# Performance work log

Measured on AMD Instinct MI355X. Metric: run time of the kernel, lower is better.

Reference implementation:

```python
import jax, jax.numpy as jnp
import numpy as np

BETA = 0.99  # EMA momentum from init_kwargs
EPS = 1e-12  # torch F.normalize eps


def _normalize(v):
    # matches torch.nn.functional.normalize (L2, dim=-1, eps clamp)
    n = jnp.maximum(jnp.linalg.norm(v, axis=-1, keepdims=True), EPS)
    return v / n


def setup_inputs() -> dict:
    key = jax.random.key(0)
    k1, k2 = jax.random.split(key)
    x = jax.random.normal(k1, (16384, 1024), dtype=jnp.float32)
    group_features = jax.random.uniform(k2, (8192, 1024), dtype=jnp.float32)
    return {"x": x, "group_features": group_features}


def reference(x, group_features):
    n_groups = group_features.shape[0]
    # assign_groups: cosine-sim argmax (normalized copies; does NOT modify x used below)
    xn = _normalize(x)
    gn = _normalize(group_features)
    logits = xn @ gn.T                      # [B, G]
    assignments = jnp.argmax(logits, axis=-1)  # [B] int

    # bincount over groups
    counts = jax.ops.segment_sum(
        jnp.ones_like(assignments, dtype=jnp.int32), assignments, num_segments=n_groups
    )  # [G]

    # scale only groups that received at least one sample by beta
    gf = jnp.where((counts > 0)[:, None], group_features * BETA, group_features)

    # scatter-add EMA contribution: (1-beta) * mean-style sum of raw x per group
    per_sample = x / counts[assignments][:, None].astype(x.dtype)  # safe: count>=1 for assigned
    contrib = jax.ops.segment_sum(per_sample, assignments, num_segments=n_groups)  # [G, D]
    gf = gf + (1.0 - BETA) * contrib

    return _normalize(gf)
```

## Files before the change

### kernel.cpp

```cpp
#include <hip/hip_runtime.h>
#include <float.h>

#define B_N 16384
#define G_N 8192
#define D_N 1024
#define NKT 48

typedef unsigned short u16;
typedef unsigned long long u64;
typedef __attribute__((ext_vector_type(8))) short short8;
typedef __attribute__((ext_vector_type(4))) float f32x4;

#define AS1 __attribute__((address_space(1)))
#define AS3 __attribute__((address_space(3)))


__global__ __launch_bounds__(256) void k_norms(const float* __restrict__ g,
                                               float* __restrict__ invn) {
    const int j = blockIdx.x;
    const int t = threadIdx.x;
    const float4 v = *reinterpret_cast<const float4*>(&g[(size_t)j * D_N + t * 4]);
    float s = v.x * v.x + v.y * v.y + v.z * v.z + v.w * v.w;
#pragma unroll
    for (int off = 32; off >= 1; off >>= 1) s += __shfl_down(s, off, 64);
    __shared__ float wsum[4];
    if ((t & 63) == 0) wsum[t >> 6] = s;
    __syncthreads();
    if (t == 0) {
        const float tot = wsum[0] + wsum[1] + wsum[2] + wsum[3];
        invn[j] = 1.0f / fmaxf(sqrtf(tot), 1e-12f);
    }
}

__global__ void k_counts(const u64* __restrict__ pk, int* __restrict__ counts) {
    const int i = blockIdx.x * blockDim.x + threadIdx.x;
    if (i < B_N) {
        const int a = 8191 - (int)(pk[i] & 0x1FFFull);
        atomicAdd(&counts[a], 1);
    }
}

__global__ __launch_bounds__(256) void k_scatter(const float* __restrict__ x,
                                                 const u64* __restrict__ pk,
                                                 const int* __restrict__ counts,
                                                 float* __restrict__ contrib) {
    const int i = blockIdx.x;
    const int a = 8191 - (int)(pk[i] & 0x1FFFull);
    const float scale = 1.0f / (float)counts[a];
    const int t = threadIdx.x;
    const float4 v = *reinterpret_cast<const float4*>(&x[(size_t)i * D_N + t * 4]);
    float* dst = &contrib[(size_t)a * D_N + t * 4];
    atomicAdd(dst + 0, v.x * scale);
    atomicAdd(dst + 1, v.y * scale);
    atomicAdd(dst + 2, v.z * scale);
    atomicAdd(dst + 3, v.w * scale);
}

__global__ __launch_bounds__(256) void k_finalize(const float* __restrict__ g,
                                                  const int* __restrict__ counts,
                                                  float* __restrict__ out) {
    const int j = blockIdx.x;
    const int t = threadIdx.x;
    const float sc = (counts[j] > 0) ? 0.99f : 1.0f;
    const float4 gv = *reinterpret_cast<const float4*>(&g[(size_t)j * D_N + t * 4]);
    const float4 cv = *reinterpret_cast<const float4*>(&out[(size_t)j * D_N + t * 4]);
    float4 gf;
    gf.x = sc * gv.x + 0.01f * cv.x;
    gf.y = sc * gv.y + 0.01f * cv.y;
    gf.z = sc * gv.z + 0.01f * cv.z;
    gf.w = sc * gv.w + 0.01f * cv.w;
    float s = gf.x * gf.x + gf.y * gf.y + gf.z * gf.z + gf.w * gf.w;
#pragma unroll
    for (int off = 32; off >= 1; off >>= 1) s += __shfl_down(s, off, 64);
    __shared__ float wsum[4];
    __shared__ float s_inv;
    if ((t & 63) == 0) wsum[t >> 6] = s;
    __syncthreads();
    if (t == 0) s_inv = 1.0f / fmaxf(sqrtf(wsum[0] + wsum[1] + wsum[2] + wsum[3]), 1e-12f);
    __syncthreads();
    gf.x *= s_inv; gf.y *= s_inv; gf.z *= s_inv; gf.w *= s_inv;
    *reinterpret_cast<float4*>(&out[(size_t)j * D_N + t * 4]) = gf;
}


__device__ inline u16 f2bf_rtn(float f) {
    unsigned u = __float_as_uint(f);
    unsigned r = u + 0x7fffu + ((u >> 16) & 1u);
    return (u16)(r >> 16);
}
__device__ inline float bf2f(u16 h) { return __uint_as_float(((unsigned)h) << 16); }

__global__ __launch_bounds__(256) void k_split(const float* __restrict__ src,
                                               u16* __restrict__ hi,
                                               u16* __restrict__ lo) {
    const size_t i4 = (size_t)blockIdx.x * 256 + threadIdx.x;
    const float4 v = *reinterpret_cast<const float4*>(&src[i4 * 4]);
    u16 h[4], l[4];
    const float f[4] = {v.x, v.y, v.z, v.w};
#pragma unroll
    for (int j = 0; j < 4; ++j) {
        h[j] = f2bf_rtn(f[j]);
        l[j] = f2bf_rtn(f[j] - bf2f(h[j]));
    }
    *reinterpret_cast<ushort4*>(&hi[i4 * 4]) = make_ushort4(h[0], h[1], h[2], h[3]);
    *reinterpret_cast<ushort4*>(&lo[i4 * 4]) = make_ushort4(l[0], l[1], l[2], l[3]);
}


#define PHASE(BUFI, Q, READB, STG, DOVM) do {                                              \
    const u16* aL = lds + (BUFI) * 32768;                                                  \
    const u16* bL = aL + 16384;                                                            \
    _Pragma("unroll")                                                                      \
    for (int dm = 0; dm < 2; ++dm) {                                                       \
        const u16* fb = aL + (wr * 8 + (Q) * 2 + dm) * 1024;                               \
        afr[dm][0] = *reinterpret_cast<const short8*>(fb + aoff0);                         \
        afr[dm][1] = *reinterpret_cast<const short8*>(fb + aoff1);                         \
    }                                                                                      \
    if (READB) {                                                                           \
        _Pragma("unroll")                                                                  \
        for (int n = 0; n < 4; ++n) {                                                      \
            const u16* fb = bL + (wc * 4 + n) * 1024;                                      \
            bfr[n][0] = *reinterpret_cast<const short8*>(fb + aoff0);                      \
            bfr[n][1] = *reinterpret_cast<const short8*>(fb + aoff1);                      \
        }                                                                                  \
    }                                                                                      \
    STG;                                                                                   \
    if (DOVM) asm volatile("s_waitcnt vmcnt(6)" ::: "memory");                             \
    __builtin_amdgcn_s_barrier();                                                          \
    asm volatile("s_waitcnt lgkmcnt(0)" ::: "memory");                                     \
    __builtin_amdgcn_s_setprio(1);                                                         \
    _Pragma("unroll")                                                                      \
    for (int s = 0; s < 2; ++s)                                                            \
        _Pragma("unroll")                                                                  \
        for (int dm = 0; dm < 2; ++dm)                                                     \
            _Pragma("unroll")                                                              \
            for (int n = 0; n < 4; ++n)                                                    \
                acc[(Q) * 2 + dm][n] = __builtin_amdgcn_mfma_f32_16x16x32_bf16(            \
                    afr[dm][s], bfr[n][s], acc[(Q) * 2 + dm][n], 0, 0, 0);                 \
    __builtin_amdgcn_s_setprio(0);                                                         \
    __builtin_amdgcn_s_barrier();                                                          \
} while (0)

__global__ __launch_bounds__(512, 2) void k_gemm_argmax(
    const u16* __restrict__ x_hi, const u16* __restrict__ x_lo,
    const u16* __restrict__ g_hi, const u16* __restrict__ g_lo,
    const float* __restrict__ invn, u64* __restrict__ pk) {

    __shared__ __align__(16) u16 lds[65536];

    const int bid = blockIdx.x;
    const int xcd = bid & 7, lcl = bid >> 3;
    const int mblk = xcd * 8 + (lcl >> 5);
    const int nblk = lcl & 31;

    const int tid = threadIdx.x;
    const int lane = tid & 63;
    const int w = tid >> 6;
    const int wr = w >> 2, wc = w & 3;
    const int mrow0 = mblk * 256;
    const int nrow0 = nblk * 256;

    const int rl = lane & 15, kg = lane >> 4;
    const int xr = rl & 7;
    const int sl0 = kg ^ xr;
    const int aoff0 = rl * 64 + (sl0 << 3);
    const int aoff1 = rl * 64 + ((sl0 ^ 4) << 3);

    const size_t soff0 = (size_t)(tid >> 3) * D_N + (size_t)(((tid & 7) ^ ((tid >> 3) & 7)) * 8);
    const size_t soff1 = soff0 + (size_t)64 * D_N;
    const int wub = (tid & 448) * 8;

    auto STGA = [&](int ktx, int half) {
        int kt = ktx < NKT ? ktx : NKT - 1;
        const u16* base = (kt >= 16 && kt < 32) ? x_lo : x_hi;
        const u16* s0 = base + (size_t)(mrow0 + half * 128) * D_N + (kt & 15) * 64;
        u16* dreg = lds + (kt & 1) * 32768 + half * 8192;
        __builtin_amdgcn_global_load_lds((const AS1 void*)(s0 + soff0), (AS3 void*)(dreg + wub), 16, 0, 0);
        __builtin_amdgcn_global_load_lds((const AS1 void*)(s0 + soff1), (AS3 void*)(dreg + wub + 4096), 16, 0, 0);
    };
    auto STGB = [&](int ktx, int half) {
        int kt = ktx < NKT ? ktx : NKT - 1;
        const u16* base = (kt < 32) ? g_hi : g_lo;
        const u16* s0 = base + (size_t)(nrow0 + half * 128) * D_N + (kt & 15) * 64;
        u16* dreg = lds + (kt & 1) * 32768 + 16384 + half * 8192;
        __builtin_amdgcn_global_load_lds((const AS1 void*)(s0 + soff0), (AS3 void*)(dreg + wub), 16, 0, 0);
        __builtin_amdgcn_global_load_lds((const AS1 void*)(s0 + soff1), (AS3 void*)(dreg + wub + 4096), 16, 0, 0);
    };

    f32x4 acc[8][4];
#pragma unroll
    for (int m = 0; m < 8; ++m)
#pragma unroll
        for (int n = 0; n < 4; ++n) acc[m][n] = (f32x4){0.f, 0.f, 0.f, 0.f};
    short8 afr[2][2], bfr[4][2];

    STGB(0, 0); STGB(0, 1); STGA(0, 0); STGA(0, 1);
    STGB(1, 0); STGB(1, 1); STGA(1, 0);
    asm volatile("s_waitcnt vmcnt(6)" ::: "memory");
    __builtin_amdgcn_s_barrier();

    for (int kt0 = 0; kt0 < NKT; kt0 += 2) {
        const int kt1 = kt0 + 1;
        PHASE(0, 0, true,  STGA(kt1, 1),     false);
        PHASE(0, 1, false, STGB(kt0 + 2, 0), false);
        PHASE(0, 2, false, STGB(kt0 + 2, 1), false);
        PHASE(0, 3, false, STGA(kt0 + 2, 0), true);
        PHASE(1, 0, true,  STGA(kt0 + 2, 1), false);
        PHASE(1, 1, false, STGB(kt1 + 2, 0), false);
        PHASE(1, 2, false, STGB(kt1 + 2, 1), false);
        PHASE(1, 3, false, STGA(kt1 + 2, 0), true);
    }

    float inv[4];
#pragma unroll
    for (int n = 0; n < 4; ++n) inv[n] = invn[nrow0 + wc * 64 + n * 16 + rl];

#pragma unroll
    for (int m = 0; m < 8; ++m) {
#pragma unroll
        for (int j = 0; j < 4; ++j) {
            u64 p = 0;
#pragma unroll
            for (int n = 0; n < 4; ++n) {
                const float v = acc[m][n][j] * inv[n];
                unsigned u = __float_as_uint(v);
                u ^= (u >> 31) ? 0xFFFFFFFFu : 0x80000000u;
                const int col = nrow0 + wc * 64 + n * 16 + rl;
                const u64 cand = ((u64)u << 13) | (unsigned)(8191 - col);
                p = (cand > p) ? cand : p;
            }
#pragma unroll
            for (int msk = 1; msk < 16; msk <<= 1) {
                const u64 o = __shfl_xor(p, msk, 64);
                p = (o > p) ? o : p;
            }
            if (rl == 0) {
                const int row = mrow0 + wr * 128 + m * 16 + kg * 4 + j;
                atomicMax(&pk[row], p);
            }
        }
    }
}


__global__ __launch_bounds__(256) void k_argmax_fp32(const float* __restrict__ x,
                                                     const float* __restrict__ g,
                                                     const float* __restrict__ invn,
                                                     int* __restrict__ assign) {
    __shared__ __align__(16) float As[32][68];
    __shared__ __align__(16) float Bs[32][68];
    const int t = threadIdx.x;
    const int tx = t & 15;
    const int ty = t >> 4;
    const int row0 = blockIdx.x * 64;
    const int r_a = t >> 3;
    const int c4 = t & 7;
    float bestv[4]; int besti[4];
#pragma unroll
    for (int i = 0; i < 4; ++i) { bestv[i] = -3.0e38f; besti[i] = 0; }
    for (int jt = 0; jt < G_N / 64; ++jt) {
        float acc[4][4] = {};
        for (int kt = 0; kt < D_N / 32; ++kt) {
#pragma unroll
            for (int p = 0; p < 2; ++p) {
                const int r = r_a + p * 32;
                const float4 va = *reinterpret_cast<const float4*>(&x[(size_t)(row0 + r) * D_N + kt * 32 + c4 * 4]);
                As[c4 * 4 + 0][r] = va.x; As[c4 * 4 + 1][r] = va.y; As[c4 * 4 + 2][r] = va.z; As[c4 * 4 + 3][r] = va.w;
                const float4 vb = *reinterpret_cast<const float4*>(&g[(size_t)(jt * 64 + r) * D_N + kt * 32 + c4 * 4]);
                Bs[c4 * 4 + 0][r] = vb.x; Bs[c4 * 4 + 1][r] = vb.y; Bs[c4 * 4 + 2][r] = vb.z; Bs[c4 * 4 + 3][r] = vb.w;
            }
            __syncthreads();
#pragma unroll
            for (int k = 0; k < 32; ++k) {
                const float4 a = *reinterpret_cast<const float4*>(&As[k][ty * 4]);
                const float4 b = *reinterpret_cast<const float4*>(&Bs[k][tx * 4]);
                const float av[4] = {a.x, a.y, a.z, a.w};
                const float bv[4] = {b.x, b.y, b.z, b.w};
#pragma unroll
                for (int i = 0; i < 4; ++i)
#pragma unroll
                    for (int jj = 0; jj < 4; ++jj) acc[i][jj] += av[i] * bv[jj];
            }
            __syncthreads();
        }
#pragma unroll
        for (int jj = 0; jj < 4; ++jj) {
            const int col = jt * 64 + tx * 4 + jj;
            const float s = invn[col];
#pragma unroll
            for (int i = 0; i < 4; ++i) {
                const float v = acc[i][jj] * s;
                if (v > bestv[i]) { bestv[i] = v; besti[i] = col; }
            }
        }
    }
#pragma unroll
    for (int m = 1; m < 16; m <<= 1) {
#pragma unroll
        for (int i = 0; i < 4; ++i) {
            const float ov = __shfl_xor(bestv[i], m, 64);
            const int oi = __shfl_xor(besti[i], m, 64);
            if (ov > bestv[i] || (ov == bestv[i] && oi < besti[i])) { bestv[i] = ov; besti[i] = oi; }
        }
    }
    if (tx == 0) {
#pragma unroll
        for (int i = 0; i < 4; ++i) assign[row0 + ty * 4 + i] = besti[i];
    }
}

__global__ void k_counts_i(const int* __restrict__ assign, int* __restrict__ counts) {
    const int i = blockIdx.x * blockDim.x + threadIdx.x;
    if (i < B_N) atomicAdd(&counts[assign[i]], 1);
}

__global__ __launch_bounds__(256) void k_scatter_i(const float* __restrict__ x,
                                                   const int* __restrict__ assign,
                                                   const int* __restrict__ counts,
                                                   float* __restrict__ contrib) {
    const int i = blockIdx.x;
    const int a = assign[i];
    const float scale = 1.0f / (float)counts[a];
    const int t = threadIdx.x;
    const float4 v = *reinterpret_cast<const float4*>(&x[(size_t)i * D_N + t * 4]);
    float* dst = &contrib[(size_t)a * D_N + t * 4];
    atomicAdd(dst + 0, v.x * scale);
    atomicAdd(dst + 1, v.y * scale);
    atomicAdd(dst + 2, v.z * scale);
    atomicAdd(dst + 3, v.w * scale);
}


extern "C" void kernel_launch(void* const* d_in, const int* in_sizes, int n_in,
                              void* d_out, int out_size, void* d_ws, size_t ws_size,
                              hipStream_t stream) {
    const float* x = (const float*)d_in[0];
    const float* g = (const float*)d_in[1];
    float* out = (float*)d_out;

    char* ws = (char*)d_ws;
    u16*  x_hi  = (u16*)(ws);
    u16*  x_lo  = (u16*)(ws + 33554432);
    u16*  g_hi  = (u16*)(ws + 67108864);
    u16*  g_lo  = (u16*)(ws + 83886080);
    float* invn = (float*)(ws + 100663296);
    int* counts = (int*)(ws + 100696064);
    u64*   pk   = (u64*)(ws + 100728832);
    const size_t need = 100859904;

    hipMemsetAsync(out, 0, (size_t)G_N * D_N * sizeof(float), stream);

    if (ws_size >= need) {
        hipMemsetAsync(counts, 0, (size_t)G_N * sizeof(int), stream);
        hipMemsetAsync(pk, 0, (size_t)B_N * sizeof(u64), stream);
        k_norms<<<G_N, 256, 0, stream>>>(g, invn);
        k_split<<<B_N * D_N / 4 / 256, 256, 0, stream>>>(x, x_hi, x_lo);
        k_split<<<G_N * D_N / 4 / 256, 256, 0, stream>>>(g, g_hi, g_lo);
        k_gemm_argmax<<<2048, 512, 0, stream>>>(x_hi, x_lo, g_hi, g_lo, invn, pk);
        k_counts<<<B_N / 256, 256, 0, stream>>>(pk, counts);
        k_scatter<<<B_N, 256, 0, stream>>>(x, pk, counts, out);
        k_finalize<<<G_N, 256, 0, stream>>>(g, counts, out);
    } else {
        float* invn_f = (float*)ws;
        int* assign_f = (int*)(ws + (size_t)G_N * 4);
        int* counts_f = (int*)(ws + (size_t)(G_N + B_N) * 4);
        hipMemsetAsync(counts_f, 0, (size_t)G_N * sizeof(int), stream);
        k_norms<<<G_N, 256, 0, stream>>>(g, invn_f);
        k_argmax_fp32<<<B_N / 64, 256, 0, stream>>>(x, g, invn_f, assign_f);
        k_counts_i<<<B_N / 256, 256, 0, stream>>>(assign_f, counts_f);
        k_scatter_i<<<B_N, 256, 0, stream>>>(x, assign_f, counts_f, out);
        k_finalize<<<G_N, 256, 0, stream>>>(g, counts_f, out);
    }
}
```

Baseline: 1.166 ms.

## Switch GEMM-argmax to 32x32x16 MFMA with triple-buffered 32-wide K pipeline

Rewrites the split-bf16 GEMM+argmax kernel main loop to use 32x32x16 bf16 MFMA instead of 16x16x32. K is staged in 32-element slices with a three-buffer LDS ring and one barrier per phase instead of two. The block-to-tile mapping is changed for better L2 locality within each XCD, and the argmax epilogue is adapted to the 32x32 accumulator layout. The aim is fewer LDS fragment reads per MFMA and less barrier overhead, at the cost of a shallower K slice per stage and new swizzle and indexing that must be exactly right.

```diff
diff --git a/kernel.cpp b/kernel.cpp
--- a/kernel.cpp
+++ b/kernel.cpp
@@ -4,12 +4,12 @@
 #define B_N 16384
 #define G_N 8192
 #define D_N 1024
-#define NKT 48
+#define NT 96
 
 typedef unsigned short u16;
 typedef unsigned long long u64;
 typedef __attribute__((ext_vector_type(8))) short short8;
-typedef __attribute__((ext_vector_type(4))) float f32x4;
+typedef __attribute__((ext_vector_type(16))) float f32x16;
 
 #define AS1 __attribute__((address_space(1)))
 #define AS3 __attribute__((address_space(3)))
@@ -107,38 +107,32 @@
 }
 
 
-#define PHASE(BUFI, Q, READB, STG, DOVM) do {                                              \
-    const u16* aL = lds + (BUFI) * 32768;                                                  \
-    const u16* bL = aL + 16384;                                                            \
-    _Pragma("unroll")                                                                      \
-    for (int dm = 0; dm < 2; ++dm) {                                                       \
-        const u16* fb = aL + (wr * 8 + (Q) * 2 + dm) * 1024;                               \
-        afr[dm][0] = *reinterpret_cast<const short8*>(fb + aoff0);                         \
-        afr[dm][1] = *reinterpret_cast<const short8*>(fb + aoff1);                         \
-    }                                                                                      \
-    if (READB) {                                                                           \
-        _Pragma("unroll")                                                                  \
-        for (int n = 0; n < 4; ++n) {                                                      \
-            const u16* fb = bL + (wc * 4 + n) * 1024;                                      \
-            bfr[n][0] = *reinterpret_cast<const short8*>(fb + aoff0);                      \
-            bfr[n][1] = *reinterpret_cast<const short8*>(fb + aoff1);                      \
-        }                                                                                  \
-    }                                                                                      \
-    STG;                                                                                   \
-    if (DOVM) asm volatile("s_waitcnt vmcnt(6)" ::: "memory");                             \
-    __builtin_amdgcn_s_barrier();                                                          \
-    asm volatile("s_waitcnt lgkmcnt(0)" ::: "memory");                                     \
-    __builtin_amdgcn_s_setprio(1);                                                         \
-    _Pragma("unroll")                                                                      \
-    for (int s = 0; s < 2; ++s)                                                            \
-        _Pragma("unroll")                                                                  \
-        for (int dm = 0; dm < 2; ++dm)                                                     \
-            _Pragma("unroll")                                                              \
-            for (int n = 0; n < 4; ++n)                                                    \
-                acc[(Q) * 2 + dm][n] = __builtin_amdgcn_mfma_f32_16x16x32_bf16(            \
-                    afr[dm][s], bfr[n][s], acc[(Q) * 2 + dm][n], 0, 0, 0);                 \
-    __builtin_amdgcn_s_setprio(0);                                                         \
-    __builtin_amdgcn_s_barrier();                                                          \
+#define PHASE(T, BUF, SBUF) do {                                                          \
+    const u16* base = lds + (BUF) * 16384;                                                \
+    short8 afr[4][2], bfr[2][2];                                                          \
+    _Pragma("unroll")                                                                     \
+    for (int m = 0; m < 4; ++m) {                                                         \
+        afr[m][0] = *reinterpret_cast<const short8*>(base + arow + m * 1024 + aoffk0);    \
+        afr[m][1] = *reinterpret_cast<const short8*>(base + arow + m * 1024 + aoffk1);    \
+    }                                                                                     \
+    _Pragma("unroll")                                                                     \
+    for (int n = 0; n < 2; ++n) {                                                         \
+        bfr[n][0] = *reinterpret_cast<const short8*>(base + brow + n * 1024 + aoffk0);    \
+        bfr[n][1] = *reinterpret_cast<const short8*>(base + brow + n * 1024 + aoffk1);    \
+    }                                                                                     \
+    STG((T) + 2, SBUF);                                                                   \
+    __builtin_amdgcn_s_setprio(1);                                                        \
+    _Pragma("unroll")                                                                     \
+    for (int ks = 0; ks < 2; ++ks)                                                        \
+        _Pragma("unroll")                                                                 \
+        for (int m = 0; m < 4; ++m)                                                       \
+            _Pragma("unroll")                                                             \
+            for (int n = 0; n < 2; ++n)                                                   \
+                acc[m][n] = __builtin_amdgcn_mfma_f32_32x32x16_bf16(                      \
+                    afr[m][ks], bfr[n][ks], acc[m][n], 0, 0, 0);                          \
+    __builtin_amdgcn_s_setprio(0);                                                        \
+    asm volatile("s_waitcnt vmcnt(4)" ::: "memory");                                      \
+    __builtin_amdgcn_s_barrier();                                                         \
 } while (0)
 
 __global__ __launch_bounds__(512, 2) void k_gemm_argmax(
@@ -146,96 +140,90 @@
     const u16* __restrict__ g_hi, const u16* __restrict__ g_lo,
     const float* __restrict__ invn, u64* __restrict__ pk) {
 
-    __shared__ __align__(16) u16 lds[65536];
+    __shared__ __align__(16) u16 lds[49152];
 
     const int bid = blockIdx.x;
     const int xcd = bid & 7, lcl = bid >> 3;
-    const int mblk = xcd * 8 + (lcl >> 5);
-    const int nblk = lcl & 31;
+    const int mblk = xcd * 8 + ((lcl >> 3) & 7);
+    const int nblk = (lcl & 7) + (lcl >> 6) * 8;
+    const int mrow0 = mblk * 256, nrow0 = nblk * 256;
 
     const int tid = threadIdx.x;
     const int lane = tid & 63;
     const int w = tid >> 6;
     const int wr = w >> 2, wc = w & 3;
-    const int mrow0 = mblk * 256;
-    const int nrow0 = nblk * 256;
-
-    const int rl = lane & 15, kg = lane >> 4;
-    const int xr = rl & 7;
-    const int sl0 = kg ^ xr;
-    const int aoff0 = rl * 64 + (sl0 << 3);
-    const int aoff1 = rl * 64 + ((sl0 ^ 4) << 3);
-
-    const size_t soff0 = (size_t)(tid >> 3) * D_N + (size_t)(((tid & 7) ^ ((tid >> 3) & 7)) * 8);
-    const size_t soff1 = soff0 + (size_t)64 * D_N;
-    const int wub = (tid & 448) * 8;
-
-    auto STGA = [&](int ktx, int half) {
-        int kt = ktx < NKT ? ktx : NKT - 1;
-        const u16* base = (kt >= 16 && kt < 32) ? x_lo : x_hi;
-        const u16* s0 = base + (size_t)(mrow0 + half * 128) * D_N + (kt & 15) * 64;
-        u16* dreg = lds + (kt & 1) * 32768 + half * 8192;
-        __builtin_amdgcn_global_load_lds((const AS1 void*)(s0 + soff0), (AS3 void*)(dreg + wub), 16, 0, 0);
-        __builtin_amdgcn_global_load_lds((const AS1 void*)(s0 + soff1), (AS3 void*)(dreg + wub + 4096), 16, 0, 0);
+
+    const int l31 = lane & 31, l5 = lane >> 5;
+    const int xq = (lane >> 1) & 3;
+    const int arow = (wr * 128 + l31) * 32;
+    const int brow = 8192 + (wc * 64 + l31) * 32;
+    const int aoffk0 = ((0 + l5) ^ xq) * 8;
+    const int aoffk1 = ((2 + l5) ^ xq) * 8;
+
+    const int r0 = tid >> 2;
+    const int xsl = (tid & 3) ^ ((tid >> 3) & 3);
+    const size_t sA = (size_t)(mrow0 + r0) * D_N + xsl * 8;
+    const size_t sB = (size_t)(nrow0 + r0) * D_N + xsl * 8;
+    const int dstc = (tid & 448) * 8;
+
+    auto STG = [&](int T, int buf3) {
+        const int Tc = T < NT ? T : NT - 1;
+        const int term = Tc >> 5;
+        const u16* xb = (term == 1) ? x_lo : x_hi;
+        const u16* gb = (term == 2) ? g_lo : g_hi;
+        const int ko = (Tc & 31) * 32;
+        u16* da = lds + buf3 * 16384;
+        u16* db = da + 8192;
+        __builtin_amdgcn_global_load_lds((const AS1 void*)(xb + sA + ko),          (AS3 void*)(da + dstc), 16, 0, 0);
+        __builtin_amdgcn_global_load_lds((const AS1 void*)(xb + sA + 131072 + ko), (AS3 void*)(da + 4096 + dstc), 16, 0, 0);
+        __builtin_amdgcn_global_load_lds((const AS1 void*)(gb + sB + ko),          (AS3 void*)(db + dstc), 16, 0, 0);
+        __builtin_amdgcn_global_load_lds((const AS1 void*)(gb + sB + 131072 + ko), (AS3 void*)(db + 4096 + dstc), 16, 0, 0);
     };
-    auto STGB = [&](int ktx, int half) {
-        int kt = ktx < NKT ? ktx : NKT - 1;
-        const u16* base = (kt < 32) ? g_hi : g_lo;
-        const u16* s0 = base + (size_t)(nrow0 + half * 128) * D_N + (kt & 15) * 64;
-        u16* dreg = lds + (kt & 1) * 32768 + 16384 + half * 8192;
-        __builtin_amdgcn_global_load_lds((const AS1 void*)(s0 + soff0), (AS3 void*)(dreg + wub), 16, 0, 0);
-        __builtin_amdgcn_global_load_lds((const AS1 void*)(s0 + soff1), (AS3 void*)(dreg + wub + 4096), 16, 0, 0);
-    };
-
-    f32x4 acc[8][4];
-#pragma unroll
-    for (int m = 0; m < 8; ++m)
-#pragma unroll
-        for (int n = 0; n < 4; ++n) acc[m][n] = (f32x4){0.f, 0.f, 0.f, 0.f};
-    short8 afr[2][2], bfr[4][2];
-
-    STGB(0, 0); STGB(0, 1); STGA(0, 0); STGA(0, 1);
-    STGB(1, 0); STGB(1, 1); STGA(1, 0);
-    asm volatile("s_waitcnt vmcnt(6)" ::: "memory");
+
+    f32x16 acc[4][2];
+#pragma unroll
+    for (int m = 0; m < 4; ++m)
+#pragma unroll
+        for (int n = 0; n < 2; ++n)
+#pragma unroll
+            for (int r = 0; r < 16; ++r) acc[m][n][r] = 0.0f;
+
+    STG(0, 0); STG(1, 1);
+    asm volatile("s_waitcnt vmcnt(4)" ::: "memory");
     __builtin_amdgcn_s_barrier();
 
-    for (int kt0 = 0; kt0 < NKT; kt0 += 2) {
-        const int kt1 = kt0 + 1;
-        PHASE(0, 0, true,  STGA(kt1, 1),     false);
-        PHASE(0, 1, false, STGB(kt0 + 2, 0), false);
-        PHASE(0, 2, false, STGB(kt0 + 2, 1), false);
-        PHASE(0, 3, false, STGA(kt0 + 2, 0), true);
-        PHASE(1, 0, true,  STGA(kt0 + 2, 1), false);
-        PHASE(1, 1, false, STGB(kt1 + 2, 0), false);
-        PHASE(1, 2, false, STGB(kt1 + 2, 1), false);
-        PHASE(1, 3, false, STGA(kt1 + 2, 0), true);
-    }
-
-    float inv[4];
-#pragma unroll
-    for (int n = 0; n < 4; ++n) inv[n] = invn[nrow0 + wc * 64 + n * 16 + rl];
-
-#pragma unroll
-    for (int m = 0; m < 8; ++m) {
-#pragma unroll
-        for (int j = 0; j < 4; ++j) {
+    for (int it = 0; it < 32; ++it) {
+        const int T = it * 3;
+        PHASE(T,     0, 2);
+        PHASE(T + 1, 1, 0);
+        PHASE(T + 2, 2, 1);
+    }
+
+    float inv[2];
+    inv[0] = invn[nrow0 + wc * 64 + l31];
+    inv[1] = invn[nrow0 + wc * 64 + 32 + l31];
+
+#pragma unroll
+    for (int m = 0; m < 4; ++m) {
+#pragma unroll
+        for (int r = 0; r < 16; ++r) {
             u64 p = 0;
 #pragma unroll
-            for (int n = 0; n < 4; ++n) {
-                const float v = acc[m][n][j] * inv[n];
+            for (int n = 0; n < 2; ++n) {
+                const float v = acc[m][n][r] * inv[n];
                 unsigned u = __float_as_uint(v);
                 u ^= (u >> 31) ? 0xFFFFFFFFu : 0x80000000u;
-                const int col = nrow0 + wc * 64 + n * 16 + rl;
+                const int col = nrow0 + wc * 64 + n * 32 + l31;
                 const u64 cand = ((u64)u << 13) | (unsigned)(8191 - col);
                 p = (cand > p) ? cand : p;
             }
 #pragma unroll
-            for (int msk = 1; msk < 16; msk <<= 1) {
+            for (int msk = 1; msk < 32; msk <<= 1) {
                 const u64 o = __shfl_xor(p, msk, 64);
                 p = (o > p) ? o : p;
             }
-            if (rl == 0) {
-                const int row = mrow0 + wr * 128 + m * 16 + kg * 4 + j;
+            if (l31 == 0) {
+                const int row = mrow0 + wr * 128 + m * 32 + (r & 3) + 8 * (r >> 2) + 4 * l5;
                 atomicMax(&pk[row], p);
             }
         }
```

After: 1.107 ms. 5.0% less time.
